# Performance work log

Hardware: AMD Instinct MI355X
Metric: run time of the kernel (lower is better)

## Reference

```python
import jax, jax.numpy as jnp
import numpy as np

N, E, F, DIM, BT, RANK = 8192, 32768, 16, 64, 4, 512
EDGE_VARIABLE = 2


def setup_inputs() -> dict:
    key = jax.random.key(0)
    ks = jax.random.split(key, 24)

    def rn(i, shape, s=0.05):
        return jax.random.normal(ks[i], shape, dtype=jnp.float32) * s

    x = jax.random.normal(ks[0], (N, F), dtype=jnp.float32)
    # first feature column is a categorical node-type id (EDGE_VARIABLE == 2)
    x = x.at[:, 0].set(jax.random.randint(ks[1], (N,), 0, 5).astype(jnp.float32))
    edge_index = jax.random.randint(ks[2], (2, E), 0, N, dtype=jnp.int32)
    edge_attr = jax.random.uniform(ks[3], (E, BT), dtype=jnp.float32)
    return {
        'x': x, 'edge_index': edge_index, 'edge_attr': edge_attr,
        'W0': rn(4, (DIM, F)), 'b0': jnp.zeros(DIM, jnp.float32),
        'nnW1': rn(5, (32, BT)), 'nnb1': jnp.zeros(32, jnp.float32),
        'nnW2': rn(6, (DIM * DIM, 32), 0.02), 'nnb2': jnp.zeros(DIM * DIM, jnp.float32),
        'root': rn(7, (DIM, DIM)), 'conv_b': jnp.zeros(DIM, jnp.float32),
        'Wih': rn(8, (3 * DIM, DIM)), 'Whh': rn(9, (3 * DIM, DIM)),
        'bih': jnp.zeros(3 * DIM, jnp.float32), 'bhh': jnp.zeros(3 * DIM, jnp.float32),
        'W1l': rn(10, (BT, DIM)), 'b1l': jnp.zeros(BT, jnp.float32),
        'WUp': rn(11, (DIM, BT)), 'bUp': jnp.zeros(DIM, jnp.float32),
        'WDown': rn(12, (BT, DIM)), 'bDown': jnp.zeros(BT, jnp.float32),
        'U': rn(13, (BT, RANK, DIM)), 'V': rn(14, (BT, DIM, RANK)),
        'weight': rn(15, (1, DIM), 1.0), 'linW': rn(16, (DIM, DIM)), 'linb': jnp.zeros(DIM, jnp.float32),
        'weight_e': rn(17, (1, BT), 1.0), 'linWe': rn(18, (BT, BT)), 'linbe': jnp.zeros(BT, jnp.float32),
    }


def _gru_cell(m, h, Wih, Whh, bih, bhh):
    # torch GRU gate order: reset, update, new
    gi = m @ Wih.T + bih
    gh = h @ Whh.T + bhh
    ir, iz, i_n = jnp.split(gi, 3, axis=-1)
    hr, hz, h_n = jnp.split(gh, 3, axis=-1)
    r = jax.nn.sigmoid(ir + hr)
    z = jax.nn.sigmoid(iz + hz)
    n = jnp.tanh(i_n + r * h_n)
    return (1.0 - z) * n + z * h


def reference(x, edge_index, edge_attr,
              W0, b0, nnW1, nnb1, nnW2, nnb2, root, conv_b,
              Wih, Whh, bih, bhh, W1l, b1l, WUp, bUp, WDown, bDown,
              U, V, weight, linW, linb, weight_e, linWe, linbe):
    n_nodes = x.shape[0]
    src, dst = edge_index[0], edge_index[1]

    out = jax.nn.relu(x @ W0.T + b0)            # [N, DIM]
    h = out

    # mean-aggregation degree (clamped)
    deg = jnp.clip(jax.ops.segment_sum(jnp.ones_like(src, dtype=out.dtype), dst,
                                       num_segments=n_nodes), 1.0)[:, None]

    # edge-conditioned per-edge weight matrices  [E, DIM, DIM]
    We = (jax.nn.relu(edge_attr @ nnW1.T + nnb1) @ nnW2.T + nnb2).reshape(-1, DIM, DIM)

    for _ in range(3):  # 3 message-passing + GRU steps
        msg = jnp.einsum('ei,eio->eo', out[src], We)                 # per-edge matvec
        agg = jax.ops.segment_sum(msg, dst, num_segments=n_nodes) / deg
        m = jax.nn.relu(out @ root + agg + conv_b)                    # NNConv(root + mean msg)
        h = _gru_cell(m, h, Wih, Whh, bih, bhh)
        out = h

    out_edges = jax.nn.relu(out @ W1l.T + b1l)                        # [N, BT]

    # combine node state with upscaled edge-variable state
    ev_mask = (x[:, 0] == EDGE_VARIABLE)
    out_combine = jnp.where(ev_mask[:, None], out_edges @ WUp.T + bUp, out)

    # FGNet factorized (rank-512) bond-type-conditioned message passing
    bond = jnp.argmax(edge_attr, axis=-1)                             # [E]
    oh = jax.nn.one_hot(bond, BT, dtype=out.dtype)                    # [E, BT]
    h_src = out_combine[src]                                          # [E, DIM]
    zf = jnp.einsum('ed,tdr->etr', h_src, V)                          # [E, BT, RANK]
    zsel = jnp.einsum('etr,et->er', zf, oh)                           # select factor by bond type
    me = jnp.einsum('er,et,trd->ed', zsel, oh, U)                     # [E, DIM]
    msg_f = jax.nn.relu(jax.ops.segment_sum(me, dst, num_segments=n_nodes) / deg)
    msg_to_edge = msg_f @ WDown.T + bDown                             # [N, BT]

    out = out + jax.nn.relu((weight * msg_f) @ linW.T + linb)
    out_edges = out_edges + jax.nn.relu((weight_e * msg_to_edge) @ linWe.T + linbe)
    return jax.nn.log_softmax(out_edges, axis=-1)
```

## Files before the change

kernel.cpp:

```cpp
#include <hip/hip_runtime.h>
#include <hip/hip_bf16.h>

#define NN 8192
#define NE 32768
#define FD 16
#define DIM 64
#define BT 4
#define RANK 512

typedef __attribute__((ext_vector_type(8))) short bf16x8;
typedef __attribute__((ext_vector_type(4))) float f32x4;

__device__ inline unsigned short f2bf(float f) {
    union { float f; unsigned u; } c; c.f = f;
    return (unsigned short)((c.u + 0x7fffu + ((c.u >> 16) & 1u)) >> 16);
}
__device__ inline float ubf(unsigned short h) {
    union { unsigned u; float f; } c; c.u = ((unsigned)h) << 16; return c.f;
}
__device__ inline float bflo(unsigned u) { union { unsigned u; float f; } c; c.u = u << 16; return c.f; }
__device__ inline float bfhi(unsigned u) { union { unsigned u; float f; } c; c.u = u & 0xffff0000u; return c.f; }

__global__ __launch_bounds__(256) void k_prep(
    const float* __restrict__ x, const int* __restrict__ ei, const float* __restrict__ ea,
    const float* __restrict__ W0, const float* __restrict__ b0,
    const float* __restrict__ nnW1, const float* __restrict__ nnb1,
    const float* __restrict__ W2, const float* __restrict__ Wih, const float* __restrict__ Whh,
    const float* __restrict__ root, const float* __restrict__ b2,
    const float* __restrict__ U, const float* __restrict__ V,
    float* __restrict__ s, unsigned short* __restrict__ shi, unsigned short* __restrict__ slo,
    float* __restrict__ deg, int* __restrict__ srccnt,
    float* __restrict__ h32, int* __restrict__ bond,
    unsigned short* __restrict__ w2h, unsigned short* __restrict__ w2l,
    unsigned short* __restrict__ wihh, unsigned short* __restrict__ wihl,
    unsigned short* __restrict__ whhh, unsigned short* __restrict__ whhl,
    unsigned short* __restrict__ rth, unsigned short* __restrict__ rtl,
    unsigned short* __restrict__ b2th, unsigned short* __restrict__ b2tl,
    float* __restrict__ M, float* __restrict__ agg)
{
    int bid = blockIdx.x, tid = threadIdx.x;
    if (bid < 512) {
#pragma unroll
        for (int q = 0; q < 4; ++q) {
            int gid = bid * 1024 + q * 256 + tid;
            int n = gid >> 6, d = gid & 63;
            const float4* xr = (const float4*)(x + (size_t)n * FD);
            const float4* wr = (const float4*)(W0 + d * FD);
            float4 x0 = xr[0], x1 = xr[1], x2 = xr[2], x3 = xr[3];
            float4 w0 = wr[0], w1 = wr[1], w2 = wr[2], w3 = wr[3];
            float acc = b0[d]
                + x0.x*w0.x + x0.y*w0.y + x0.z*w0.z + x0.w*w0.w
                + x1.x*w1.x + x1.y*w1.y + x1.z*w1.z + x1.w*w1.w
                + x2.x*w2.x + x2.y*w2.y + x2.z*w2.z + x2.w*w2.w
                + x3.x*w3.x + x3.y*w3.y + x3.z*w3.z + x3.w*w3.w;
            float sv = fmaxf(acc, 0.f);
            s[gid] = sv;
            unsigned short h = f2bf(sv);
            shi[gid] = h; slo[gid] = f2bf(sv - ubf(h));
        }
    } else if (bid < 1536) {
        int eb = (bid - 512) * 32;
#pragma unroll
        for (int p = 0; p < 4; ++p) {
            int e = eb + p * 8 + (tid >> 5);
            int k = tid & 31;
            float a0 = ea[e * 4 + 0], a1 = ea[e * 4 + 1], a2 = ea[e * 4 + 2], a3 = ea[e * 4 + 3];
            float h = nnb1[k] + a0 * nnW1[k * 4 + 0] + a1 * nnW1[k * 4 + 1]
                              + a2 * nnW1[k * 4 + 2] + a3 * nnW1[k * 4 + 3];
            h32[e * 32 + k] = fmaxf(h, 0.f);
            if (k == 0) {
                int bi = 0; float bv = a0;
                if (a1 > bv) { bv = a1; bi = 1; }
                if (a2 > bv) { bv = a2; bi = 2; }
                if (a3 > bv) { bv = a3; bi = 3; }
                bond[e] = bi;
                atomicAdd(&deg[ei[NE + e]], 1.0f);
                atomicAdd(&srccnt[ei[e]], 1);
            }
        }
    } else if (bid < 1664) {
#pragma unroll
        for (int q = 0; q < 4; ++q) {
            int gid = (bid - 1536) * 1024 + q * 256 + tid;
            int col = gid >> 6, i = gid & 63;
            float v = W2[(size_t)(i * 64 + (col >> 5)) * 32 + (col & 31)];
            unsigned short h = f2bf(v);
            w2h[gid] = h; w2l[gid] = f2bf(v - ubf(h));
        }
    } else if (bid < 1688) {
#pragma unroll
        for (int q = 0; q < 4; ++q) {
            int gid = (bid - 1664) * 1024 + q * 256 + tid;
            if (gid < 12288) {
                float v = Wih[gid];
                unsigned short h = f2bf(v);
                wihh[gid] = h; wihl[gid] = f2bf(v - ubf(h));
            } else {
                int g = gid - 12288;
                float v = Whh[g];
                unsigned short h = f2bf(v);
                whhh[g] = h; whhl[g] = f2bf(v - ubf(h));
            }
        }
    } else if (bid < 1696) {
#pragma unroll
        for (int q = 0; q < 4; ++q) {
            int gid = (bid - 1688) * 1024 + q * 256 + tid;
            if (gid < 4096) {
                int o = gid >> 6, i = gid & 63;
                float v = root[i * 64 + o];
                unsigned short h = f2bf(v);
                rth[gid] = h; rtl[gid] = f2bf(v - ubf(h));
            } else {
                int g = gid - 4096;
                int o = g >> 6, i = g & 63;
                float v = b2[i * 64 + o];
                unsigned short h = f2bf(v);
                b2th[g] = h; b2tl[g] = f2bf(v - ubf(h));
            }
        }
    } else if (bid < 1952) {
        __shared__ float red[4][64];
        int t = bid - 1696;
        int b = t >> 6, d = t & 63;
        int chunk = tid >> 6, dp = tid & 63;
        const float* Vp = V + ((size_t)b * DIM + d) * RANK;
        const float* Up = U + (size_t)b * RANK * DIM;
        float acc = 0.f;
        for (int r = chunk * 128; r < chunk * 128 + 128; ++r)
            acc += Vp[r] * Up[(size_t)r * DIM + dp];
        red[chunk][dp] = acc;
        __syncthreads();
        if (chunk == 0)
            M[((size_t)b * DIM + d) * DIM + dp] =
                red[0][dp] + red[1][dp] + red[2][dp] + red[3][dp];
    } else {
        float4* zp = ((float4*)agg) + (size_t)(bid - 1952) * 4096;
#pragma unroll
        for (int q = 0; q < 16; ++q)
            zp[q * 256 + tid] = make_float4(0.f, 0.f, 0.f, 0.f);
    }
}

__global__ __launch_bounds__(1024) void k_scan(const int* __restrict__ cnt,
                                               int* __restrict__ start, int* __restrict__ cursor) {
    __shared__ int wsum[16];
    int tid = threadIdx.x, lane = tid & 63, wv = tid >> 6;
    int v[8], tot = 0;
#pragma unroll
    for (int j = 0; j < 8; ++j) { v[j] = cnt[tid * 8 + j]; tot += v[j]; }
    int incl = tot;
#pragma unroll
    for (int off = 1; off < 64; off <<= 1) {
        int t = __shfl_up(incl, off);
        if (lane >= off) incl += t;
    }
    if (lane == 63) wsum[wv] = incl;
    __syncthreads();
    if (wv == 0) {
        int wval = (lane < 16) ? wsum[lane] : 0;
        int winc = wval;
#pragma unroll
        for (int off = 1; off < 16; off <<= 1) {
            int t = __shfl_up(winc, off);
            if (lane >= off) winc += t;
        }
        if (lane < 16) wsum[lane] = winc - wval;
    }
    __syncthreads();
    int run = wsum[wv] + incl - tot;
#pragma unroll
    for (int j = 0; j < 8; ++j) {
        start[tid * 8 + j] = run; cursor[tid * 8 + j] = run; run += v[j];
    }
    if (tid == 1023) start[NN] = run;
}

__global__ __launch_bounds__(256) void k_scatter(const int* __restrict__ ei,
                                                 int* __restrict__ cursor, int* __restrict__ eord) {
    int e = blockIdx.x * 256 + threadIdx.x;
    int pos = atomicAdd(&cursor[ei[e]], 1);
    eord[pos] = e;
}

__global__ __launch_bounds__(256) void k_gemm_A(const unsigned short* __restrict__ sh,
                                                const unsigned short* __restrict__ sl,
                                                const unsigned short* __restrict__ wh,
                                                const unsigned short* __restrict__ wl,
                                                const unsigned short* __restrict__ b2th,
                                                const unsigned short* __restrict__ b2tl,
                                                unsigned short* __restrict__ A,
                                                float* __restrict__ cbuf) {
    int tid = threadIdx.x, wid = tid >> 6, lane = tid & 63;
    int lr = lane & 15, kg = lane >> 4;
    if (blockIdx.y == 16) {
        int rbase = blockIdx.x * 128 + wid * 32;
        f32x4 acc[2][4] = {};
#pragma unroll
        for (int kb = 0; kb < 2; ++kb) {
            bf16x8 ah[2], al[2];
#pragma unroll
            for (int mi = 0; mi < 2; ++mi) {
                size_t off = (size_t)(rbase + mi * 16 + lr) * 64 + kb * 32 + kg * 8;
                ah[mi] = *(const bf16x8*)(sh + off);
                al[mi] = *(const bf16x8*)(sl + off);
            }
#pragma unroll
            for (int ni = 0; ni < 4; ++ni) {
                size_t offB = (size_t)(ni * 16 + lr) * 64 + kb * 32 + kg * 8;
                bf16x8 bh = *(const bf16x8*)(b2th + offB);
                bf16x8 bl = *(const bf16x8*)(b2tl + offB);
#pragma unroll
                for (int mi = 0; mi < 2; ++mi) {
                    acc[mi][ni] = __builtin_amdgcn_mfma_f32_16x16x32_bf16(ah[mi], bh, acc[mi][ni], 0, 0, 0);
                    acc[mi][ni] = __builtin_amdgcn_mfma_f32_16x16x32_bf16(ah[mi], bl, acc[mi][ni], 0, 0, 0);
                    acc[mi][ni] = __builtin_amdgcn_mfma_f32_16x16x32_bf16(al[mi], bh, acc[mi][ni], 0, 0, 0);
                }
            }
        }
#pragma unroll
        for (int mi = 0; mi < 2; ++mi)
#pragma unroll
            for (int r = 0; r < 4; ++r)
#pragma unroll
                for (int ni = 0; ni < 4; ++ni)
                    cbuf[(size_t)(rbase + mi * 16 + kg * 4 + r) * 64 + ni * 16 + lr] = acc[mi][ni][r];
        return;
    }
    int mbase = blockIdx.x * 128 + (wid >> 1) * 64;
    int nbase = blockIdx.y * 128 + (wid & 1) * 64;
    f32x4 acc[4][4] = {};
#pragma unroll
    for (int kb = 0; kb < 2; ++kb) {
        bf16x8 ah[4], al[4], bh[4], bl[4];
#pragma unroll
        for (int mi = 0; mi < 4; ++mi) {
            size_t off = (size_t)(mbase + mi * 16 + lr) * 64 + kb * 32 + kg * 8;
            ah[mi] = *(const bf16x8*)(sh + off);
            al[mi] = *(const bf16x8*)(sl + off);
        }
#pragma unroll
        for (int ni = 0; ni < 4; ++ni) {
            size_t off = (size_t)(nbase + ni * 16 + lr) * 64 + kb * 32 + kg * 8;
            bh[ni] = *(const bf16x8*)(wh + off);
            bl[ni] = *(const bf16x8*)(wl + off);
        }
#pragma unroll
        for (int mi = 0; mi < 4; ++mi)
#pragma unroll
            for (int ni = 0; ni < 4; ++ni) {
                acc[mi][ni] = __builtin_amdgcn_mfma_f32_16x16x32_bf16(ah[mi], bh[ni], acc[mi][ni], 0, 0, 0);
                acc[mi][ni] = __builtin_amdgcn_mfma_f32_16x16x32_bf16(ah[mi], bl[ni], acc[mi][ni], 0, 0, 0);
                acc[mi][ni] = __builtin_amdgcn_mfma_f32_16x16x32_bf16(al[mi], bh[ni], acc[mi][ni], 0, 0, 0);
            }
    }
#pragma unroll
    for (int mi = 0; mi < 4; ++mi)
#pragma unroll
        for (int r = 0; r < 4; ++r) {
            size_t row = (size_t)(mbase + mi * 16 + kg * 4 + r) * 2048;
#pragma unroll
            for (int ni = 0; ni < 4; ++ni)
                A[row + nbase + ni * 16 + lr] = f2bf(acc[mi][ni][r]);
        }
}

__global__ __launch_bounds__(256) void k_edge(const int* __restrict__ ei,
                                              const int* __restrict__ startp,
                                              const int* __restrict__ srccnt,
                                              const int* __restrict__ eord,
                                              const float* __restrict__ h32,
                                              const unsigned short* __restrict__ A,
                                              const float* __restrict__ cbuf,
                                              float* __restrict__ agg) {
    int tid = threadIdx.x, wid = tid >> 6, o = tid & 63;
    int n = blockIdx.x * 4 + wid;
    int cnt = srccnt[n];
    if (cnt == 0) return;
    int beg = startp[n];
    float cv = cbuf[(size_t)n * DIM + o];
    const uint4* Ap = (const uint4*)(A + (size_t)n * 2048 + o * 32);
    uint4 a0 = Ap[0], a1 = Ap[1], a2 = Ap[2], a3 = Ap[3];
    for (int i = beg; i < beg + cnt; ++i) {
        int e = eord[i];
        int dst = ei[NE + e];
        const float4* hp = (const float4*)(h32 + (size_t)e * 32);
        float acc = cv;
        float4 hA = hp[0], hB = hp[1];
        acc += hA.x*bflo(a0.x) + hA.y*bfhi(a0.x) + hA.z*bflo(a0.y) + hA.w*bfhi(a0.y)
             + hB.x*bflo(a0.z) + hB.y*bfhi(a0.z) + hB.z*bflo(a0.w) + hB.w*bfhi(a0.w);
        hA = hp[2]; hB = hp[3];
        acc += hA.x*bflo(a1.x) + hA.y*bfhi(a1.x) + hA.z*bflo(a1.y) + hA.w*bfhi(a1.y)
             + hB.x*bflo(a1.z) + hB.y*bfhi(a1.z) + hB.z*bflo(a1.w) + hB.w*bfhi(a1.w);
        hA = hp[4]; hB = hp[5];
        acc += hA.x*bflo(a2.x) + hA.y*bfhi(a2.x) + hA.z*bflo(a2.y) + hA.w*bfhi(a2.y)
             + hB.x*bflo(a2.z) + hB.y*bfhi(a2.z) + hB.z*bflo(a2.w) + hB.w*bfhi(a2.w);
        hA = hp[6]; hB = hp[7];
        acc += hA.x*bflo(a3.x) + hA.y*bfhi(a3.x) + hA.z*bflo(a3.y) + hA.w*bfhi(a3.y)
             + hB.x*bflo(a3.z) + hB.y*bfhi(a3.z) + hB.z*bflo(a3.w) + hB.w*bfhi(a3.w);
        atomicAdd(&agg[(size_t)dst * DIM + o], acc);
    }
}

__global__ __launch_bounds__(256) void k_upd(
    float* __restrict__ s, unsigned short* __restrict__ shi, unsigned short* __restrict__ slo,
    float* __restrict__ agg, const float* __restrict__ deg, const float* __restrict__ conv_b,
    const unsigned short* __restrict__ rth, const unsigned short* __restrict__ rtl,
    const unsigned short* __restrict__ wihh, const unsigned short* __restrict__ wihl,
    const unsigned short* __restrict__ whhh, const unsigned short* __restrict__ whhl,
    const float* __restrict__ bih, const float* __restrict__ bhh,
    const float* __restrict__ x, const float* __restrict__ W1l, const float* __restrict__ b1l,
    const float* __restrict__ WUp, const float* __restrict__ bUp,
    float* __restrict__ oe, float* __restrict__ oc, int last)
{
    __shared__ unsigned short mh_l[16 * 64];
    __shared__ unsigned short ml_l[16 * 64];
    __shared__ float gl[16 * 384];
    __shared__ float oel[64];
    int tid = threadIdx.x;
    int wid = tid >> 6, lane = tid & 63;
    int lr = lane & 15, kg = lane >> 4;
    int m0 = blockIdx.x * 16;

    bf16x8 sa_h[2], sa_l[2];
#pragma unroll
    for (int kb = 0; kb < 2; ++kb) {
        size_t off = (size_t)(m0 + lr) * 64 + kb * 32 + kg * 8;
        sa_h[kb] = *(const bf16x8*)(shi + off);
        sa_l[kb] = *(const bf16x8*)(slo + off);
    }

    f32x4 macc = {};
#pragma unroll
    for (int kb = 0; kb < 2; ++kb) {
        size_t offB = (size_t)(wid * 16 + lr) * 64 + kb * 32 + kg * 8;
        bf16x8 bh = *(const bf16x8*)(rth + offB);
        bf16x8 bl = *(const bf16x8*)(rtl + offB);
        macc = __builtin_amdgcn_mfma_f32_16x16x32_bf16(sa_h[kb], bh, macc, 0, 0, 0);
        macc = __builtin_amdgcn_mfma_f32_16x16x32_bf16(sa_h[kb], bl, macc, 0, 0, 0);
        macc = __builtin_amdgcn_mfma_f32_16x16x32_bf16(sa_l[kb], bh, macc, 0, 0, 0);
    }
#pragma unroll
    for (int r = 0; r < 4; ++r) {
        int row = m0 + kg * 4 + r;
        float inv = 1.f / fmaxf(deg[row], 1.f);
        int col = wid * 16 + lr;
        size_t idx = (size_t)row * 64 + col;
        float v = macc[r] + agg[idx] * inv + conv_b[col];
        agg[idx] = 0.f;
        v = fmaxf(v, 0.f);
        unsigned short h = f2bf(v);
        int loff = (kg * 4 + r) * 64 + col;
        mh_l[loff] = h; ml_l[loff] = f2bf(v - ubf(h));
    }
    __syncthreads();

    bf16x8 ma_h[2], ma_l[2];
#pragma unroll
    for (int kb = 0; kb < 2; ++kb) {
        int loff = lr * 64 + kb * 32 + kg * 8;
        ma_h[kb] = *(const bf16x8*)(mh_l + loff);
        ma_l[kb] = *(const bf16x8*)(ml_l + loff);
    }
    f32x4 gacc[3] = {}, hacc[3] = {};
#pragma unroll
    for (int kb = 0; kb < 2; ++kb)
#pragma unroll
        for (int j = 0; j < 3; ++j) {
            int ni = wid * 3 + j;
            size_t offB = (size_t)(ni * 16 + lr) * 64 + kb * 32 + kg * 8;
            bf16x8 bh = *(const bf16x8*)(wihh + offB);
            bf16x8 bl = *(const bf16x8*)(wihl + offB);
            gacc[j] = __builtin_amdgcn_mfma_f32_16x16x32_bf16(ma_h[kb], bh, gacc[j], 0, 0, 0);
            gacc[j] = __builtin_amdgcn_mfma_f32_16x16x32_bf16(ma_h[kb], bl, gacc[j], 0, 0, 0);
            gacc[j] = __builtin_amdgcn_mfma_f32_16x16x32_bf16(ma_l[kb], bh, gacc[j], 0, 0, 0);
            bf16x8 ch = *(const bf16x8*)(whhh + offB);
            bf16x8 cl = *(const bf16x8*)(whhl + offB);
            hacc[j] = __builtin_amdgcn_mfma_f32_16x16x32_bf16(sa_h[kb], ch, hacc[j], 0, 0, 0);
            hacc[j] = __builtin_amdgcn_mfma_f32_16x16x32_bf16(sa_h[kb], cl, hacc[j], 0, 0, 0);
            hacc[j] = __builtin_amdgcn_mfma_f32_16x16x32_bf16(sa_l[kb], ch, hacc[j], 0, 0, 0);
        }
#pragma unroll
    for (int j = 0; j < 3; ++j)
#pragma unroll
        for (int r = 0; r < 4; ++r) {
            int row = kg * 4 + r;
            int col = (wid * 3 + j) * 16 + lr;
            gl[row * 384 + col] = gacc[j][r];
            gl[row * 384 + 192 + col] = hacc[j][r];
        }
    __syncthreads();

#pragma unroll
    for (int k = 0; k < 4; ++k) {
        int item = tid + k * 256;
        int row = item >> 6, d = item & 63;
        size_t idx = (size_t)(m0 + row) * 64 + d;
        const float* gr = gl + row * 384;
        float ir = gr[d], iz = gr[64 + d], in_ = gr[128 + d];
        float hr_ = gr[192 + d], hz = gr[256 + d], hn = gr[320 + d];
        float hv = s[idx];
        float rg = 1.f / (1.f + expf(-(ir + bih[d] + hr_ + bhh[d])));
        float z  = 1.f / (1.f + expf(-(iz + bih[64 + d] + hz + bhh[64 + d])));
        float nv = tanhf(in_ + bih[128 + d] + rg * (hn + bhh[128 + d]));
        float nh = (1.f - z) * nv + z * hv;
        if (!last) {
            s[idx] = nh;
            unsigned short hb = f2bf(nh);
            shi[idx] = hb; slo[idx] = f2bf(nh - ubf(hb));
        }
        gl[row * 384 + d] = nh;
    }
    if (!last) return;
    __syncthreads();

    {
        int node16 = tid >> 4, j = tid & 15, t = j & 3, q = j >> 2;
        float p = 0.f;
#pragma unroll
        for (int i = 0; i < 16; ++i)
            p += gl[node16 * 384 + q * 16 + i] * W1l[t * 64 + q * 16 + i];
        p += __shfl_xor(p, 4);
        p += __shfl_xor(p, 8);
        if (q == 0) {
            float v = fmaxf(p + b1l[t], 0.f);
            oel[node16 * 4 + t] = v;
            oe[(size_t)(m0 + node16) * 4 + t] = v;
        }
    }
    __syncthreads();
#pragma unroll
    for (int k = 0; k < 4; ++k) {
        int item = tid + k * 256;
        int row = item >> 6, d = item & 63;
        int node = m0 + row;
        float sval = gl[row * 384 + d];
        float ocv;
        if (x[(size_t)node * FD] == 2.0f) {
            ocv = bUp[d];
#pragma unroll
            for (int t = 0; t < 4; ++t) ocv += oel[row * 4 + t] * WUp[d * 4 + t];
        } else {
            ocv = sval;
        }
        oc[(size_t)node * DIM + d] = ocv;
    }
}

__global__ __launch_bounds__(256) void k_fgedge(const int* __restrict__ ei,
                                                const int* __restrict__ bond,
                                                const float* __restrict__ oc,
                                                const float* __restrict__ M,
                                                float* __restrict__ fg_agg) {
    __shared__ float so[4][64];
    int tid = threadIdx.x, w = tid >> 6, lane = tid & 63;
    int e = blockIdx.x * 4 + w;
    int src = ei[e], dst = ei[NE + e];
    int b = bond[e];
    so[w][lane] = oc[(size_t)src * DIM + lane];
    __syncthreads();
    float acc = 0.f;
    const float* Mp = M + b * DIM * DIM;
    for (int d = 0; d < 64; ++d) acc += so[w][d] * Mp[d * 64 + lane];
    atomicAdd(&fg_agg[(size_t)dst * DIM + lane], acc);
}

__global__ __launch_bounds__(256) void k_final(const float* __restrict__ fg_agg,
                                               const float* __restrict__ deg,
                                               const float* __restrict__ oe,
                                               const float* __restrict__ WDown,
                                               const float* __restrict__ bDown,
                                               const float* __restrict__ weight_e,
                                               const float* __restrict__ linWe,
                                               const float* __restrict__ linbe,
                                               float* __restrict__ out) {
    int tid = threadIdx.x, w = tid >> 6, lane = tid & 63;
    int node = blockIdx.x * 4 + w;
    float degc = fmaxf(deg[node], 1.f);
    float mf = fmaxf(fg_agg[(size_t)node * DIM + lane] / degc, 0.f);
    float mte[4];
#pragma unroll
    for (int t = 0; t < 4; ++t) {
        float p = mf * WDown[t * 64 + lane];
#pragma unroll
        for (int off = 32; off; off >>= 1) p += __shfl_xor(p, off);
        mte[t] = p + bDown[t];
    }
    float val[4];
    float mx = -1e30f;
#pragma unroll
    for (int t = 0; t < 4; ++t) {
        float acc = linbe[t];
#pragma unroll
        for (int t2 = 0; t2 < 4; ++t2) acc += weight_e[t2] * mte[t2] * linWe[t * 4 + t2];
        val[t] = oe[(size_t)node * 4 + t] + fmaxf(acc, 0.f);
        mx = fmaxf(mx, val[t]);
    }
    float lse = 0.f;
#pragma unroll
    for (int t = 0; t < 4; ++t) lse += expf(val[t] - mx);
    lse = logf(lse);
    if (lane < 4) out[(size_t)node * 4 + lane] = val[lane] - mx - lse;
}

extern "C" void kernel_launch(void* const* d_in, const int* in_sizes, int n_in,
                              void* d_out, int out_size, void* d_ws, size_t ws_size,
                              hipStream_t stream) {
    const float* x       = (const float*)d_in[0];
    const int*   ei      = (const int*)  d_in[1];
    const float* ea      = (const float*)d_in[2];
    const float* W0      = (const float*)d_in[3];
    const float* b0      = (const float*)d_in[4];
    const float* nnW1    = (const float*)d_in[5];
    const float* nnb1    = (const float*)d_in[6];
    const float* nnW2    = (const float*)d_in[7];
    const float* nnb2    = (const float*)d_in[8];
    const float* root    = (const float*)d_in[9];
    const float* conv_b  = (const float*)d_in[10];
    const float* Wih     = (const float*)d_in[11];
    const float* Whh     = (const float*)d_in[12];
    const float* bih     = (const float*)d_in[13];
    const float* bhh     = (const float*)d_in[14];
    const float* W1l     = (const float*)d_in[15];
    const float* b1l     = (const float*)d_in[16];
    const float* WUp     = (const float*)d_in[17];
    const float* bUp     = (const float*)d_in[18];
    const float* WDown   = (const float*)d_in[19];
    const float* bDown   = (const float*)d_in[20];
    const float* U       = (const float*)d_in[21];
    const float* V       = (const float*)d_in[22];
    const float* weight_e= (const float*)d_in[26];
    const float* linWe   = (const float*)d_in[27];
    const float* linbe   = (const float*)d_in[28];
    float* out = (float*)d_out;

    char* ws = (char*)d_ws;
    size_t off = 0;
    auto alloc = [&](size_t bytes) { size_t o = off; off = (off + bytes + 255) & ~(size_t)255; return o; };
    float* deg    = (float*)(ws + alloc((size_t)NN * 4));
    int*   srccnt = (int*)  (ws + alloc((size_t)NN * 4));
    float* agg    = (float*)(ws + alloc((size_t)NN * DIM * 4));
    float* fg_agg = (float*)(ws + alloc((size_t)NN * DIM * 4));
    float* s      = (float*)(ws + alloc((size_t)NN * DIM * 4));
    unsigned short* shi = (unsigned short*)(ws + alloc((size_t)NN * DIM * 2));
    unsigned short* slo = (unsigned short*)(ws + alloc((size_t)NN * DIM * 2));
    float* cbuf   = (float*)(ws + alloc((size_t)NN * DIM * 4));
    float* h32    = (float*)(ws + alloc((size_t)NE * 32 * 4));
    int*   bond   = (int*)  (ws + alloc((size_t)NE * 4));
    int*   startp = (int*)  (ws + alloc((size_t)(NN + 1) * 4));
    int*   cursor = (int*)  (ws + alloc((size_t)NN * 4));
    int*   eord   = (int*)  (ws + alloc((size_t)NE * 4));
    float* oe     = (float*)(ws + alloc((size_t)NN * 4 * 4));
    float* oc     = (float*)(ws + alloc((size_t)NN * DIM * 4));
    float* Mbuf   = (float*)(ws + alloc((size_t)BT * DIM * DIM * 4));
    unsigned short* w2h = (unsigned short*)(ws + alloc((size_t)2048 * 64 * 2));
    unsigned short* w2l = (unsigned short*)(ws + alloc((size_t)2048 * 64 * 2));
    unsigned short* wihh = (unsigned short*)(ws + alloc((size_t)192 * 64 * 2));
    unsigned short* wihl = (unsigned short*)(ws + alloc((size_t)192 * 64 * 2));
    unsigned short* whhh = (unsigned short*)(ws + alloc((size_t)192 * 64 * 2));
    unsigned short* whhl = (unsigned short*)(ws + alloc((size_t)192 * 64 * 2));
    unsigned short* rth  = (unsigned short*)(ws + alloc((size_t)64 * 64 * 2));
    unsigned short* rtl  = (unsigned short*)(ws + alloc((size_t)64 * 64 * 2));
    unsigned short* b2th = (unsigned short*)(ws + alloc((size_t)64 * 64 * 2));
    unsigned short* b2tl = (unsigned short*)(ws + alloc((size_t)64 * 64 * 2));
    unsigned short* Abuf = (unsigned short*)(ws + alloc((size_t)NN * 2048 * 2));
    (void)n_in; (void)in_sizes; (void)out_size; (void)ws_size;

    hipMemsetAsync(deg, 0, (size_t)2 * NN * 4, stream);

    k_prep<<<2016, 256, 0, stream>>>(x, ei, ea, W0, b0, nnW1, nnb1,
                                     nnW2, Wih, Whh, root, nnb2, U, V,
                                     s, shi, slo, deg, srccnt, h32, bond,
                                     w2h, w2l, wihh, wihl, whhh, whhl,
                                     rth, rtl, b2th, b2tl, Mbuf, agg);
    k_scan<<<1, 1024, 0, stream>>>(srccnt, startp, cursor);
    k_scatter<<<NE / 256, 256, 0, stream>>>(ei, cursor, eord);

    for (int it = 0; it < 3; ++it) {
        k_gemm_A<<<dim3(NN / 128, 17), 256, 0, stream>>>(shi, slo, w2h, w2l, b2th, b2tl,
                                                         Abuf, cbuf);
        k_edge<<<NN / 4, 256, 0, stream>>>(ei, startp, srccnt, eord, h32, Abuf, cbuf, agg);
        k_upd<<<NN / 16, 256, 0, stream>>>(s, shi, slo, agg, deg, conv_b,
                                           rth, rtl, wihh, wihl, whhh, whhl, bih, bhh,
                                           x, W1l, b1l, WUp, bUp, oe, oc, it == 2);
    }

    k_fgedge<<<NE / 4, 256, 0, stream>>>(ei, bond, oc, Mbuf, fg_agg);
    k_final<<<NN / 4, 256, 0, stream>>>(fg_agg, deg, oe, WDown, bDown, weight_e, linWe, linbe, out);
}
```

Measured before the change: 231.0 us.

## Fuse next-iteration A/cbuf GEMM into GRU update and merge scan with scatter

The per-iteration k_gemm_A launch is removed for iterations 2 and 3. Each k_upd block now computes the new hidden state's projection onto w2 (the A buffer) and b2t (cbuf) with MFMA, reading the split-bf16 state it just produced from shared memory, so the state is not re-read from global and two launches are saved. The scan and scatter kernels are also merged into one single-block kernel that uses shared-memory cursors. The risk is that k_upd does much more work per block (2048 output columns with only 512 blocks), and the scatter now runs on one block, which serialises 32K atomics.

```diff
diff --git a/kernel.cpp b/kernel.cpp
--- a/kernel.cpp
+++ b/kernel.cpp
@@ -142,8 +142,11 @@
     }
 }
 
-__global__ __launch_bounds__(1024) void k_scan(const int* __restrict__ cnt,
-                                               int* __restrict__ start, int* __restrict__ cursor) {
+__global__ __launch_bounds__(1024) void k_scansc(const int* __restrict__ cnt,
+                                                 const int* __restrict__ ei,
+                                                 int* __restrict__ startp,
+                                                 int* __restrict__ eord) {
+    __shared__ int lcur[NN];
     __shared__ int wsum[16];
     int tid = threadIdx.x, lane = tid & 63, wv = tid >> 6;
     int v[8], tot = 0;
@@ -171,16 +174,14 @@
     int run = wsum[wv] + incl - tot;
 #pragma unroll
     for (int j = 0; j < 8; ++j) {
-        start[tid * 8 + j] = run; cursor[tid * 8 + j] = run; run += v[j];
-    }
-    if (tid == 1023) start[NN] = run;
-}
-
-__global__ __launch_bounds__(256) void k_scatter(const int* __restrict__ ei,
-                                                 int* __restrict__ cursor, int* __restrict__ eord) {
-    int e = blockIdx.x * 256 + threadIdx.x;
-    int pos = atomicAdd(&cursor[ei[e]], 1);
-    eord[pos] = e;
+        startp[tid * 8 + j] = run; lcur[tid * 8 + j] = run; run += v[j];
+    }
+    if (tid == 1023) startp[NN] = run;
+    __syncthreads();
+    for (int e = tid; e < NE; e += 1024) {
+        int pos = atomicAdd(&lcur[ei[e]], 1);
+        eord[pos] = e;
+    }
 }
 
 __global__ __launch_bounds__(256) void k_gemm_A(const unsigned short* __restrict__ sh,
@@ -311,12 +312,17 @@
     const float* __restrict__ bih, const float* __restrict__ bhh,
     const float* __restrict__ x, const float* __restrict__ W1l, const float* __restrict__ b1l,
     const float* __restrict__ WUp, const float* __restrict__ bUp,
-    float* __restrict__ oe, float* __restrict__ oc, int last)
+    float* __restrict__ oe, float* __restrict__ oc,
+    const unsigned short* __restrict__ w2h, const unsigned short* __restrict__ w2l,
+    const unsigned short* __restrict__ b2th, const unsigned short* __restrict__ b2tl,
+    unsigned short* __restrict__ A, float* __restrict__ cbuf, int last)
 {
     __shared__ unsigned short mh_l[16 * 64];
     __shared__ unsigned short ml_l[16 * 64];
     __shared__ float gl[16 * 384];
     __shared__ float oel[64];
+    __shared__ unsigned short nh_h[16 * 64];
+    __shared__ unsigned short nh_l[16 * 64];
     int tid = threadIdx.x;
     int wid = tid >> 6, lane = tid & 63;
     int lr = lane & 15, kg = lane >> 4;
@@ -404,46 +410,89 @@
         float z  = 1.f / (1.f + expf(-(iz + bih[64 + d] + hz + bhh[64 + d])));
         float nv = tanhf(in_ + bih[128 + d] + rg * (hn + bhh[128 + d]));
         float nh = (1.f - z) * nv + z * hv;
+        unsigned short hb = f2bf(nh);
+        unsigned short lb = f2bf(nh - ubf(hb));
         if (!last) {
             s[idx] = nh;
-            unsigned short hb = f2bf(nh);
-            shi[idx] = hb; slo[idx] = f2bf(nh - ubf(hb));
+            shi[idx] = hb; slo[idx] = lb;
+            nh_h[row * 64 + d] = hb; nh_l[row * 64 + d] = lb;
         }
         gl[row * 384 + d] = nh;
     }
-    if (!last) return;
     __syncthreads();
 
+    if (last) {
+        {
+            int node16 = tid >> 4, j = tid & 15, t = j & 3, q = j >> 2;
+            float p = 0.f;
+#pragma unroll
+            for (int i = 0; i < 16; ++i)
+                p += gl[node16 * 384 + q * 16 + i] * W1l[t * 64 + q * 16 + i];
+            p += __shfl_xor(p, 4);
+            p += __shfl_xor(p, 8);
+            if (q == 0) {
+                float v = fmaxf(p + b1l[t], 0.f);
+                oel[node16 * 4 + t] = v;
+                oe[(size_t)(m0 + node16) * 4 + t] = v;
+            }
+        }
+        __syncthreads();
+#pragma unroll
+        for (int k = 0; k < 4; ++k) {
+            int item = tid + k * 256;
+            int row = item >> 6, d = item & 63;
+            int node = m0 + row;
+            float sval = gl[row * 384 + d];
+            float ocv;
+            if (x[(size_t)node * FD] == 2.0f) {
+                ocv = bUp[d];
+#pragma unroll
+                for (int t = 0; t < 4; ++t) ocv += oel[row * 4 + t] * WUp[d * 4 + t];
+            } else {
+                ocv = sval;
+            }
+            oc[(size_t)node * DIM + d] = ocv;
+        }
+        return;
+    }
+
+    bf16x8 na_h[2], na_l[2];
+#pragma unroll
+    for (int kb = 0; kb < 2; ++kb) {
+        int loff = lr * 64 + kb * 32 + kg * 8;
+        na_h[kb] = *(const bf16x8*)(nh_h + loff);
+        na_l[kb] = *(const bf16x8*)(nh_l + loff);
+    }
+    for (int t = 0; t < 32; ++t) {
+        int ncol = (wid * 32 + t) * 16;
+        f32x4 acc = {};
+#pragma unroll
+        for (int kb = 0; kb < 2; ++kb) {
+            size_t offB = (size_t)(ncol + lr) * 64 + kb * 32 + kg * 8;
+            bf16x8 bh = *(const bf16x8*)(w2h + offB);
+            bf16x8 bl = *(const bf16x8*)(w2l + offB);
+            acc = __builtin_amdgcn_mfma_f32_16x16x32_bf16(na_h[kb], bh, acc, 0, 0, 0);
+            acc = __builtin_amdgcn_mfma_f32_16x16x32_bf16(na_h[kb], bl, acc, 0, 0, 0);
+            acc = __builtin_amdgcn_mfma_f32_16x16x32_bf16(na_l[kb], bh, acc, 0, 0, 0);
+        }
+#pragma unroll
+        for (int r = 0; r < 4; ++r)
+            A[(size_t)(m0 + kg * 4 + r) * 2048 + ncol + lr] = f2bf(acc[r]);
+    }
     {
-        int node16 = tid >> 4, j = tid & 15, t = j & 3, q = j >> 2;
-        float p = 0.f;
-#pragma unroll
-        for (int i = 0; i < 16; ++i)
-            p += gl[node16 * 384 + q * 16 + i] * W1l[t * 64 + q * 16 + i];
-        p += __shfl_xor(p, 4);
-        p += __shfl_xor(p, 8);
-        if (q == 0) {
-            float v = fmaxf(p + b1l[t], 0.f);
-            oel[node16 * 4 + t] = v;
-            oe[(size_t)(m0 + node16) * 4 + t] = v;
-        }
-    }
-    __syncthreads();
-#pragma unroll
-    for (int k = 0; k < 4; ++k) {
-        int item = tid + k * 256;
-        int row = item >> 6, d = item & 63;
-        int node = m0 + row;
-        float sval = gl[row * 384 + d];
-        float ocv;
-        if (x[(size_t)node * FD] == 2.0f) {
-            ocv = bUp[d];
-#pragma unroll
-            for (int t = 0; t < 4; ++t) ocv += oel[row * 4 + t] * WUp[d * 4 + t];
-        } else {
-            ocv = sval;
-        }
-        oc[(size_t)node * DIM + d] = ocv;
+        f32x4 cacc = {};
+#pragma unroll
+        for (int kb = 0; kb < 2; ++kb) {
+            size_t offB = (size_t)(wid * 16 + lr) * 64 + kb * 32 + kg * 8;
+            bf16x8 bh = *(const bf16x8*)(b2th + offB);
+            bf16x8 bl = *(const bf16x8*)(b2tl + offB);
+            cacc = __builtin_amdgcn_mfma_f32_16x16x32_bf16(na_h[kb], bh, cacc, 0, 0, 0);
+            cacc = __builtin_amdgcn_mfma_f32_16x16x32_bf16(na_h[kb], bl, cacc, 0, 0, 0);
+            cacc = __builtin_amdgcn_mfma_f32_16x16x32_bf16(na_l[kb], bh, cacc, 0, 0, 0);
+        }
+#pragma unroll
+        for (int r = 0; r < 4; ++r)
+            cbuf[(size_t)(m0 + kg * 4 + r) * 64 + wid * 16 + lr] = cacc[r];
     }
 }
 
@@ -548,7 +597,6 @@
     float* h32    = (float*)(ws + alloc((size_t)NE * 32 * 4));
     int*   bond   = (int*)  (ws + alloc((size_t)NE * 4));
     int*   startp = (int*)  (ws + alloc((size_t)(NN + 1) * 4));
-    int*   cursor = (int*)  (ws + alloc((size_t)NN * 4));
     int*   eord   = (int*)  (ws + alloc((size_t)NE * 4));
     float* oe     = (float*)(ws + alloc((size_t)NN * 4 * 4));
     float* oc     = (float*)(ws + alloc((size_t)NN * DIM * 4));
@@ -573,16 +621,16 @@
                                      s, shi, slo, deg, srccnt, h32, bond,
                                      w2h, w2l, wihh, wihl, whhh, whhl,
                                      rth, rtl, b2th, b2tl, Mbuf, agg);
-    k_scan<<<1, 1024, 0, stream>>>(srccnt, startp, cursor);
-    k_scatter<<<NE / 256, 256, 0, stream>>>(ei, cursor, eord);
-
+    k_scansc<<<1, 1024, 0, stream>>>(srccnt, ei, startp, eord);
+
+    k_gemm_A<<<dim3(NN / 128, 17), 256, 0, stream>>>(shi, slo, w2h, w2l, b2th, b2tl,
+                                                     Abuf, cbuf);
     for (int it = 0; it < 3; ++it) {
-        k_gemm_A<<<dim3(NN / 128, 17), 256, 0, stream>>>(shi, slo, w2h, w2l, b2th, b2tl,
-                                                         Abuf, cbuf);
         k_edge<<<NN / 4, 256, 0, stream>>>(ei, startp, srccnt, eord, h32, Abuf, cbuf, agg);
         k_upd<<<NN / 16, 256, 0, stream>>>(s, shi, slo, agg, deg, conv_b,
                                            rth, rtl, wihh, wihl, whhh, whhl, bih, bhh,
-                                           x, W1l, b1l, WUp, bUp, oe, oc, it == 2);
+                                           x, W1l, b1l, WUp, bUp, oe, oc,
+                                           w2h, w2l, b2th, b2tl, Abuf, cbuf, it == 2);
     }
 
     k_fgedge<<<NE / 4, 256, 0, stream>>>(ei, bond, oc, Mbuf, fg_agg);
```

After: 264.2 us. 1.14x slower.
